# Performance work log

Hardware: AMD Instinct MI355X
Metric: run time of the kernel (lower is better)

## Reference

```python
import jax, jax.numpy as jnp
import numpy as np

N_NODES, D_NODE = 100000, 128
N_EDGES, D_EDGE = 1000000, 32
D_IN = 2 * D_NODE + D_EDGE  # 288
H1, H2, D_OUT = 128, 64, 1


def setup_inputs() -> dict:
    key = jax.random.key(0)
    ks = jax.random.split(key, 9)
    x = jax.random.normal(ks[0], (N_NODES, D_NODE), dtype=jnp.float32)
    edge_index = jax.random.randint(ks[1], (2, N_EDGES), 0, N_NODES, dtype=jnp.int64)
    edge_features = jax.random.normal(ks[2], (N_EDGES, D_EDGE), dtype=jnp.float32)
    def lin(kw, kb, fan_in, fan_out):
        bound = 1.0 / np.sqrt(fan_in)
        W = jax.random.uniform(kw, (fan_in, fan_out), minval=-bound, maxval=bound, dtype=jnp.float32)
        b = jax.random.uniform(kb, (fan_out,), minval=-bound, maxval=bound, dtype=jnp.float32)
        return W, b
    W1, b1 = lin(ks[3], ks[4], D_IN, H1)
    W2, b2 = lin(ks[5], ks[6], H1, H2)
    W3, b3 = lin(ks[7], ks[8], H2, D_OUT)
    return {"x": x, "edge_index": edge_index, "edge_features": edge_features,
            "W1": W1, "b1": b1, "W2": W2, "b2": b2, "W3": W3, "b3": b3}


def reference(x, edge_index, edge_features, W1, b1, W2, b2, W3, b3):
    origin, destination = edge_index[0], edge_index[1]
    # [E, 2*D_NODE + D_EDGE]
    z = jnp.concatenate([x[origin], x[destination], edge_features], axis=1)
    z = jax.nn.leaky_relu(z @ W1 + b1)  # negative_slope=0.01, matches torch default
    z = jax.nn.leaky_relu(z @ W2 + b2)
    z = z @ W3 + b3
    return z.reshape(-1)
```

## Files before the change

### kernel.cpp

```cpp
#include <hip/hip_runtime.h>

#define N_NODES 100000
#define N_EDGES 1000000

typedef __attribute__((ext_vector_type(8))) short bf16x8;
typedef __attribute__((ext_vector_type(4))) float f32x4;

static __device__ __forceinline__ short f2bf(float f) {
    unsigned u = __float_as_uint(f);
    u = (u + 0x7fffu + ((u >> 16) & 1u)) >> 16;
    return (short)u;
}
static __device__ __forceinline__ float bf2f(unsigned short s) {
    return __uint_as_float(((unsigned)s) << 16);
}
static __device__ __forceinline__ float lrelu(float x) {
    return fmaxf(x, 0.01f * x);
}

__global__ __launch_bounds__(256) void precompute_mfma(
    const float* __restrict__ x, const float* __restrict__ W1,
    const float* __restrict__ b1, unsigned short* __restrict__ Pb,
    unsigned short* __restrict__ Qb)
{
    const int t    = threadIdx.x;
    const int lane = t & 63;
    const int w    = t >> 6;
    const int q    = lane >> 4;
    const int n15  = lane & 15;
    const int chb  = 64 * w;

    bf16x8 afrag[4][4];
    #pragma unroll
    for (int mtl = 0; mtl < 4; ++mtl) {
        const int ch = chb + 16 * mtl + n15;
        const float* wcol = (ch < 128) ? (W1 + ch) : (W1 + 128 * 128 + (ch - 128));
        #pragma unroll
        for (int ks = 0; ks < 4; ++ks)
            #pragma unroll
            for (int j = 0; j < 8; ++j)
                afrag[mtl][ks][j] = f2bf(wcol[(size_t)(32 * ks + 8 * q + j) * 128]);
    }
    float b1r[16];
    #pragma unroll
    for (int mtl = 0; mtl < 4; ++mtl)
        #pragma unroll
        for (int r = 0; r < 4; ++r) {
            const int ch = chb + 16 * mtl + 4 * q + r;
            b1r[mtl * 4 + r] = (ch < 128) ? b1[ch] : 0.0f;
        }

    unsigned short* tbase = (w < 2) ? Pb : Qb;
    const int mtb = 4 * (w & 1);

    for (int tile = blockIdx.x; tile < N_NODES / 16; tile += gridDim.x) {
        const int n0 = tile * 16;
        const float* xrow = x + (size_t)(n0 + n15) * 128;

        bf16x8 bfr[4];
        #pragma unroll
        for (int ks = 0; ks < 4; ++ks) {
            f32x4 xa = *(const f32x4*)(xrow + 32 * ks + 8 * q);
            f32x4 xb = *(const f32x4*)(xrow + 32 * ks + 8 * q + 4);
            #pragma unroll
            for (int j = 0; j < 4; ++j) { bfr[ks][j] = f2bf(xa[j]); bfr[ks][4 + j] = f2bf(xb[j]); }
        }
        #pragma unroll
        for (int mtl = 0; mtl < 4; ++mtl) {
            f32x4 acc = {0.f, 0.f, 0.f, 0.f};
            #pragma unroll
            for (int ks = 0; ks < 4; ++ks)
                acc = __builtin_amdgcn_mfma_f32_16x16x32_bf16(afrag[mtl][ks], bfr[ks], acc, 0, 0, 0);
            unsigned short hs[4];
            #pragma unroll
            for (int r = 0; r < 4; ++r) hs[r] = (unsigned short)f2bf(acc[r] + b1r[mtl * 4 + r]);
            unsigned* dst = (unsigned*)(tbase + (size_t)(n0 + n15) * 128 + q * 32 + (mtb + mtl) * 4);
            dst[0] = (unsigned)hs[0] | ((unsigned)hs[1] << 16);
            dst[1] = (unsigned)hs[2] | ((unsigned)hs[3] << 16);
        }
    }
}

__global__ __launch_bounds__(256, 2) void edge_mfma(
    const int* __restrict__ ei, const float* __restrict__ ef,
    const float* __restrict__ W1, const float* __restrict__ W2,
    const float* __restrict__ b2, const float* __restrict__ W3,
    const float* __restrict__ b3, const unsigned short* __restrict__ Pb,
    const unsigned short* __restrict__ Qb, float* __restrict__ out)
{
    __shared__ unsigned short hbuf[4][16 * 136 + 8];
    const int t    = threadIdx.x;
    const int lane = t & 63;
    const int w    = t >> 6;
    const int q    = lane >> 4;
    const int n15  = lane & 15;
    unsigned short* hb = &hbuf[w][0];

    bf16x8 a1[8];
    #pragma unroll
    for (int mt = 0; mt < 8; ++mt)
        #pragma unroll
        for (int j = 0; j < 8; ++j)
            a1[mt][j] = f2bf(W1[(size_t)(256 + 8 * q + j) * 128 + 16 * mt + n15]);

    bf16x8 a2[4][4];
    #pragma unroll
    for (int mt2 = 0; mt2 < 4; ++mt2)
        #pragma unroll
        for (int ks = 0; ks < 4; ++ks)
            #pragma unroll
            for (int j = 0; j < 8; ++j)
                a2[mt2][ks][j] = f2bf(W2[(size_t)(32 * ks + 8 * q + j) * 64 + 16 * mt2 + n15]);

    unsigned b2w3[16];
    #pragma unroll
    for (int mt2 = 0; mt2 < 4; ++mt2)
        #pragma unroll
        for (int r = 0; r < 4; ++r) {
            const int ch = 16 * mt2 + 4 * q + r;
            b2w3[mt2 * 4 + r] = (unsigned)(unsigned short)f2bf(b2[ch])
                              | ((unsigned)(unsigned short)f2bf(W3[ch]) << 16);
        }
    const float b3v = b3[0];

    const int nTiles  = N_EDGES / 16;
    const int wid     = blockIdx.x * 4 + w;
    const int wstride = gridDim.x * 4;
    if (wid >= nTiles) return;

    int tile = wid;
    int e0   = tile * 16;
    int oi = ei[e0 + n15];
    int di = ei[N_EDGES + e0 + n15];
    f32x4 ea = *(const f32x4*)(ef + (size_t)(e0 + n15) * 32 + 8 * q);
    f32x4 eb = *(const f32x4*)(ef + (size_t)(e0 + n15) * 32 + 8 * q + 4);
    bf16x8 pvb[4], qvb[4];
    {
        const unsigned short* prow = Pb + (size_t)oi * 128 + q * 32;
        const unsigned short* qrow = Qb + (size_t)di * 128 + q * 32;
        #pragma unroll
        for (int c = 0; c < 4; ++c) {
            pvb[c] = *(const bf16x8*)(prow + 8 * c);
            qvb[c] = *(const bf16x8*)(qrow + 8 * c);
        }
    }

    while (true) {
        const int  next = tile + wstride;
        const bool have = next < nTiles;

        bf16x8 bef;
        #pragma unroll
        for (int j = 0; j < 4; ++j) { bef[j] = f2bf(ea[j]); bef[4 + j] = f2bf(eb[j]); }

        int noi = 0, ndi = 0;
        f32x4 nea = ea, neb = eb;
        if (have) {
            const int ne0 = next * 16;
            noi = ei[ne0 + n15];
            ndi = ei[N_EDGES + ne0 + n15];
            nea = *(const f32x4*)(ef + (size_t)(ne0 + n15) * 32 + 8 * q);
            neb = *(const f32x4*)(ef + (size_t)(ne0 + n15) * 32 + 8 * q + 4);
        }

        #pragma unroll
        for (int mt = 0; mt < 8; ++mt) {
            f32x4 z = {0.f, 0.f, 0.f, 0.f};
            f32x4 h = __builtin_amdgcn_mfma_f32_16x16x32_bf16(a1[mt], bef, z, 0, 0, 0);
            const int c = mt >> 1, off = (mt & 1) * 4;
            unsigned short hs[4];
            #pragma unroll
            for (int r = 0; r < 4; ++r) {
                float v = h[r] + bf2f((unsigned short)pvb[c][off + r])
                               + bf2f((unsigned short)qvb[c][off + r]);
                hs[r] = (unsigned short)f2bf(lrelu(v));
            }
            unsigned* d = (unsigned*)&hb[n15 * 136 + 16 * mt + 4 * q];
            d[0] = (unsigned)hs[0] | ((unsigned)hs[1] << 16);
            d[1] = (unsigned)hs[2] | ((unsigned)hs[3] << 16);
        }

        if (have) {
            const unsigned short* prow = Pb + (size_t)noi * 128 + q * 32;
            const unsigned short* qrow = Qb + (size_t)ndi * 128 + q * 32;
            #pragma unroll
            for (int c = 0; c < 4; ++c) {
                pvb[c] = *(const bf16x8*)(prow + 8 * c);
                qvb[c] = *(const bf16x8*)(qrow + 8 * c);
            }
        }

        __asm__ __volatile__("s_waitcnt lgkmcnt(0)" ::: "memory");

        f32x4 acc2[4] = {{0.f,0.f,0.f,0.f},{0.f,0.f,0.f,0.f},{0.f,0.f,0.f,0.f},{0.f,0.f,0.f,0.f}};
        #pragma unroll
        for (int ks = 0; ks < 4; ++ks) {
            bf16x8 hfrag = *(const bf16x8*)&hb[n15 * 136 + 32 * ks + 8 * q];
            #pragma unroll
            for (int mt2 = 0; mt2 < 4; ++mt2)
                acc2[mt2] = __builtin_amdgcn_mfma_f32_16x16x32_bf16(a2[mt2][ks], hfrag, acc2[mt2], 0, 0, 0);
        }

        float s = 0.0f;
        #pragma unroll
        for (int mt2 = 0; mt2 < 4; ++mt2)
            #pragma unroll
            for (int r = 0; r < 4; ++r) {
                const unsigned u = b2w3[mt2 * 4 + r];
                float v = acc2[mt2][r] + bf2f((unsigned short)(u & 0xffffu));
                v = lrelu(v);
                s += v * __uint_as_float(u & 0xffff0000u);
            }
        s += __shfl_xor(s, 16);
        s += __shfl_xor(s, 32);
        if (q == 0) out[e0 + n15] = s + b3v;

        if (!have) break;
        tile = next;
        e0   = next * 16;
        oi = noi; di = ndi; ea = nea; eb = neb;
    }
}

extern "C" void kernel_launch(void* const* d_in, const int* in_sizes, int n_in,
                              void* d_out, int out_size, void* d_ws, size_t ws_size,
                              hipStream_t stream) {
    const float* x   = (const float*)d_in[0];
    const int*   ei  = (const int*)d_in[1];
    const float* ef  = (const float*)d_in[2];
    const float* W1  = (const float*)d_in[3];
    const float* b1  = (const float*)d_in[4];
    const float* W2  = (const float*)d_in[5];
    const float* b2  = (const float*)d_in[6];
    const float* W3  = (const float*)d_in[7];
    const float* b3  = (const float*)d_in[8];
    float*       out = (float*)d_out;

    unsigned short* Pb = (unsigned short*)d_ws;
    unsigned short* Qb = Pb + (size_t)N_NODES * 128;

    precompute_mfma<<<2048, 256, 0, stream>>>(x, W1, b1, Pb, Qb);
    edge_mfma<<<1536, 256, 0, stream>>>(ei, ef, W1, W2, b2, W3, b3, Pb, Qb, out);
}
```

Measured before the change: 343.3 us.

## Move W2 fragments to LDS, deepen prefetch, raise occupancy, use packed bf16 converts

The W2 MFMA fragments now live in shared memory instead of per-thread registers, which frees VGPRs so launch bounds can target 3 blocks per CU. The grid changes from 1536 to 1024 blocks. Edge indices and features are prefetched two tiles ahead instead of one, to hide more gather latency. Manual bf16 rounding is replaced by the packed v_cvt_pk_bf16_f32 instruction. In exchange, the second layer adds LDS reads for every MFMA and a block-wide barrier at setup.

After: 354.8 us. 3.3% more time.

```diff
diff --git a/kernel.cpp b/kernel.cpp
--- a/kernel.cpp
+++ b/kernel.cpp
@@ -5,6 +5,7 @@
 
 typedef __attribute__((ext_vector_type(8))) short bf16x8;
 typedef __attribute__((ext_vector_type(4))) float f32x4;
+typedef __attribute__((ext_vector_type(4))) unsigned u32x4;
 
 static __device__ __forceinline__ short f2bf(float f) {
     unsigned u = __float_as_uint(f);
@@ -16,6 +17,11 @@
 }
 static __device__ __forceinline__ float lrelu(float x) {
     return fmaxf(x, 0.01f * x);
+}
+static __device__ __forceinline__ unsigned cvtpk(float lo, float hi) {
+    unsigned r;
+    asm("v_cvt_pk_bf16_f32 %0, %1, %2" : "=v"(r) : "v"(lo), "v"(hi));
+    return r;
 }
 
 __global__ __launch_bounds__(256) void precompute_mfma(
@@ -62,8 +68,12 @@
         for (int ks = 0; ks < 4; ++ks) {
             f32x4 xa = *(const f32x4*)(xrow + 32 * ks + 8 * q);
             f32x4 xb = *(const f32x4*)(xrow + 32 * ks + 8 * q + 4);
-            #pragma unroll
-            for (int j = 0; j < 4; ++j) { bfr[ks][j] = f2bf(xa[j]); bfr[ks][4 + j] = f2bf(xb[j]); }
+            u32x4 bu;
+            bu[0] = cvtpk(xa[0], xa[1]);
+            bu[1] = cvtpk(xa[2], xa[3]);
+            bu[2] = cvtpk(xb[0], xb[1]);
+            bu[3] = cvtpk(xb[2], xb[3]);
+            bfr[ks] = __builtin_bit_cast(bf16x8, bu);
         }
         #pragma unroll
         for (int mtl = 0; mtl < 4; ++mtl) {
@@ -71,17 +81,14 @@
             #pragma unroll
             for (int ks = 0; ks < 4; ++ks)
                 acc = __builtin_amdgcn_mfma_f32_16x16x32_bf16(afrag[mtl][ks], bfr[ks], acc, 0, 0, 0);
-            unsigned short hs[4];
-            #pragma unroll
-            for (int r = 0; r < 4; ++r) hs[r] = (unsigned short)f2bf(acc[r] + b1r[mtl * 4 + r]);
             unsigned* dst = (unsigned*)(tbase + (size_t)(n0 + n15) * 128 + q * 32 + (mtb + mtl) * 4);
-            dst[0] = (unsigned)hs[0] | ((unsigned)hs[1] << 16);
-            dst[1] = (unsigned)hs[2] | ((unsigned)hs[3] << 16);
-        }
-    }
-}
-
-__global__ __launch_bounds__(256, 2) void edge_mfma(
+            dst[0] = cvtpk(acc[0] + b1r[mtl * 4 + 0], acc[1] + b1r[mtl * 4 + 1]);
+            dst[1] = cvtpk(acc[2] + b1r[mtl * 4 + 2], acc[3] + b1r[mtl * 4 + 3]);
+        }
+    }
+}
+
+__global__ __launch_bounds__(256, 3) void edge_mfma(
     const int* __restrict__ ei, const float* __restrict__ ef,
     const float* __restrict__ W1, const float* __restrict__ W2,
     const float* __restrict__ b2, const float* __restrict__ W3,
@@ -89,6 +96,7 @@
     const unsigned short* __restrict__ Qb, float* __restrict__ out)
 {
     __shared__ unsigned short hbuf[4][16 * 136 + 8];
+    __shared__ unsigned short w2s[16 * 64 * 8];
     const int t    = threadIdx.x;
     const int lane = t & 63;
     const int w    = t >> 6;
@@ -103,14 +111,17 @@
         for (int j = 0; j < 8; ++j)
             a1[mt][j] = f2bf(W1[(size_t)(256 + 8 * q + j) * 128 + 16 * mt + n15]);
 
-    bf16x8 a2[4][4];
-    #pragma unroll
-    for (int mt2 = 0; mt2 < 4; ++mt2)
-        #pragma unroll
-        for (int ks = 0; ks < 4; ++ks)
+    {
+        const int mt2 = w;
+        #pragma unroll
+        for (int ks = 0; ks < 4; ++ks) {
+            bf16x8 f;
             #pragma unroll
             for (int j = 0; j < 8; ++j)
-                a2[mt2][ks][j] = f2bf(W2[(size_t)(32 * ks + 8 * q + j) * 64 + 16 * mt2 + n15]);
+                f[j] = f2bf(W2[(size_t)(32 * ks + 8 * q + j) * 64 + 16 * mt2 + n15]);
+            *(bf16x8*)&w2s[(((mt2 << 2) | ks) * 64 + lane) * 8] = f;
+        }
+    }
 
     unsigned b2w3[16];
     #pragma unroll
@@ -123,21 +134,37 @@
         }
     const float b3v = b3[0];
 
+    __syncthreads();
+
     const int nTiles  = N_EDGES / 16;
     const int wid     = blockIdx.x * 4 + w;
     const int wstride = gridDim.x * 4;
     if (wid >= nTiles) return;
 
-    int tile = wid;
-    int e0   = tile * 16;
-    int oi = ei[e0 + n15];
-    int di = ei[N_EDGES + e0 + n15];
-    f32x4 ea = *(const f32x4*)(ef + (size_t)(e0 + n15) * 32 + 8 * q);
-    f32x4 eb = *(const f32x4*)(ef + (size_t)(e0 + n15) * 32 + 8 * q + 4);
+    int tile0 = wid;
+    int tile1 = tile0 + wstride;
+    bool have1 = tile1 < nTiles;
+
+    int oi0, di0; f32x4 ea0, eb0;
+    {
+        const int e0 = tile0 * 16;
+        oi0 = ei[e0 + n15];
+        di0 = ei[N_EDGES + e0 + n15];
+        ea0 = *(const f32x4*)(ef + (size_t)(e0 + n15) * 32 + 8 * q);
+        eb0 = *(const f32x4*)(ef + (size_t)(e0 + n15) * 32 + 8 * q + 4);
+    }
+    int oi1 = 0, di1 = 0; f32x4 ea1 = ea0, eb1 = eb0;
+    if (have1) {
+        const int e1 = tile1 * 16;
+        oi1 = ei[e1 + n15];
+        di1 = ei[N_EDGES + e1 + n15];
+        ea1 = *(const f32x4*)(ef + (size_t)(e1 + n15) * 32 + 8 * q);
+        eb1 = *(const f32x4*)(ef + (size_t)(e1 + n15) * 32 + 8 * q + 4);
+    }
     bf16x8 pvb[4], qvb[4];
     {
-        const unsigned short* prow = Pb + (size_t)oi * 128 + q * 32;
-        const unsigned short* qrow = Qb + (size_t)di * 128 + q * 32;
+        const unsigned short* prow = Pb + (size_t)oi0 * 128 + q * 32;
+        const unsigned short* qrow = Qb + (size_t)di0 * 128 + q * 32;
         #pragma unroll
         for (int c = 0; c < 4; ++c) {
             pvb[c] = *(const bf16x8*)(prow + 8 * c);
@@ -146,21 +173,22 @@
     }
 
     while (true) {
-        const int  next = tile + wstride;
-        const bool have = next < nTiles;
-
-        bf16x8 bef;
-        #pragma unroll
-        for (int j = 0; j < 4; ++j) { bef[j] = f2bf(ea[j]); bef[4 + j] = f2bf(eb[j]); }
-
-        int noi = 0, ndi = 0;
-        f32x4 nea = ea, neb = eb;
-        if (have) {
-            const int ne0 = next * 16;
-            noi = ei[ne0 + n15];
-            ndi = ei[N_EDGES + ne0 + n15];
-            nea = *(const f32x4*)(ef + (size_t)(ne0 + n15) * 32 + 8 * q);
-            neb = *(const f32x4*)(ef + (size_t)(ne0 + n15) * 32 + 8 * q + 4);
+        u32x4 befu;
+        befu[0] = cvtpk(ea0[0], ea0[1]);
+        befu[1] = cvtpk(ea0[2], ea0[3]);
+        befu[2] = cvtpk(eb0[0], eb0[1]);
+        befu[3] = cvtpk(eb0[2], eb0[3]);
+        const bf16x8 bef = __builtin_bit_cast(bf16x8, befu);
+
+        const int  tile2 = tile1 + wstride;
+        const bool have2 = have1 && (tile2 < nTiles);
+        int oi2 = oi1, di2 = di1; f32x4 ea2 = ea1, eb2 = eb1;
+        if (have2) {
+            const int e2 = tile2 * 16;
+            oi2 = ei[e2 + n15];
+            di2 = ei[N_EDGES + e2 + n15];
+            ea2 = *(const f32x4*)(ef + (size_t)(e2 + n15) * 32 + 8 * q);
+            eb2 = *(const f32x4*)(ef + (size_t)(e2 + n15) * 32 + 8 * q + 4);
         }
 
         #pragma unroll
@@ -168,21 +196,18 @@
             f32x4 z = {0.f, 0.f, 0.f, 0.f};
             f32x4 h = __builtin_amdgcn_mfma_f32_16x16x32_bf16(a1[mt], bef, z, 0, 0, 0);
             const int c = mt >> 1, off = (mt & 1) * 4;
-            unsigned short hs[4];
-            #pragma unroll
-            for (int r = 0; r < 4; ++r) {
-                float v = h[r] + bf2f((unsigned short)pvb[c][off + r])
-                               + bf2f((unsigned short)qvb[c][off + r]);
-                hs[r] = (unsigned short)f2bf(lrelu(v));
-            }
+            float v0 = lrelu(h[0] + bf2f((unsigned short)pvb[c][off + 0]) + bf2f((unsigned short)qvb[c][off + 0]));
+            float v1 = lrelu(h[1] + bf2f((unsigned short)pvb[c][off + 1]) + bf2f((unsigned short)qvb[c][off + 1]));
+            float v2 = lrelu(h[2] + bf2f((unsigned short)pvb[c][off + 2]) + bf2f((unsigned short)qvb[c][off + 2]));
+            float v3 = lrelu(h[3] + bf2f((unsigned short)pvb[c][off + 3]) + bf2f((unsigned short)qvb[c][off + 3]));
             unsigned* d = (unsigned*)&hb[n15 * 136 + 16 * mt + 4 * q];
-            d[0] = (unsigned)hs[0] | ((unsigned)hs[1] << 16);
-            d[1] = (unsigned)hs[2] | ((unsigned)hs[3] << 16);
-        }
-
-        if (have) {
-            const unsigned short* prow = Pb + (size_t)noi * 128 + q * 32;
-            const unsigned short* qrow = Qb + (size_t)ndi * 128 + q * 32;
+            d[0] = cvtpk(v0, v1);
+            d[1] = cvtpk(v2, v3);
+        }
+
+        if (have1) {
+            const unsigned short* prow = Pb + (size_t)oi1 * 128 + q * 32;
+            const unsigned short* qrow = Qb + (size_t)di1 * 128 + q * 32;
             #pragma unroll
             for (int c = 0; c < 4; ++c) {
                 pvb[c] = *(const bf16x8*)(prow + 8 * c);
@@ -195,10 +220,12 @@
         f32x4 acc2[4] = {{0.f,0.f,0.f,0.f},{0.f,0.f,0.f,0.f},{0.f,0.f,0.f,0.f},{0.f,0.f,0.f,0.f}};
         #pragma unroll
         for (int ks = 0; ks < 4; ++ks) {
-            bf16x8 hfrag = *(const bf16x8*)&hb[n15 * 136 + 32 * ks + 8 * q];
-            #pragma unroll
-            for (int mt2 = 0; mt2 < 4; ++mt2)
-                acc2[mt2] = __builtin_amdgcn_mfma_f32_16x16x32_bf16(a2[mt2][ks], hfrag, acc2[mt2], 0, 0, 0);
+            const bf16x8 hfrag = *(const bf16x8*)&hb[n15 * 136 + 32 * ks + 8 * q];
+            #pragma unroll
+            for (int mt2 = 0; mt2 < 4; ++mt2) {
+                const bf16x8 a2f = *(const bf16x8*)&w2s[(((mt2 << 2) | ks) * 64 + lane) * 8];
+                acc2[mt2] = __builtin_amdgcn_mfma_f32_16x16x32_bf16(a2f, hfrag, acc2[mt2], 0, 0, 0);
+            }
         }
 
         float s = 0.0f;
@@ -213,12 +240,12 @@
             }
         s += __shfl_xor(s, 16);
         s += __shfl_xor(s, 32);
-        if (q == 0) out[e0 + n15] = s + b3v;
-
-        if (!have) break;
-        tile = next;
-        e0   = next * 16;
-        oi = noi; di = ndi; ea = nea; eb = neb;
+        if (q == 0) out[tile0 * 16 + n15] = s + b3v;
+
+        if (!have1) break;
+        tile0 = tile1; tile1 = tile2; have1 = have2;
+        oi1 = oi2; di1 = di2;
+        ea0 = ea1; eb0 = eb1; ea1 = ea2; eb1 = eb2;
     }
 }
 
@@ -240,5 +267,5 @@
     unsigned short* Qb = Pb + (size_t)N_NODES * 128;
 
     precompute_mfma<<<2048, 256, 0, stream>>>(x, W1, b1, Pb, Qb);
-    edge_mfma<<<1536, 256, 0, stream>>>(ei, ef, W1, W2, b2, W3, b3, Pb, Qb, out);
-}
+    edge_mfma<<<1024, 256, 0, stream>>>(ei, ef, W1, W2, b2, W3, b3, Pb, Qb, out);
+}
```
